# Kernel tuning notes

Measured on AMD Instinct MI355X. Metric: run time of the kernel, lower is better.

The kernel has to match this reference:

```python
import jax, jax.numpy as jnp
import numpy as np

BS, S, D, N, E = 16, 8, 10, 32, 300
H, STATE_DIM, MID, OC = 128, 96, 256, 100

def setup_inputs():
    ks = jax.random.split(jax.random.key(0), 24)
    g = lambda i, shape: (0.02 * jax.random.normal(ks[i], shape)).astype(jnp.float32)
    return {
        "stock_news": jax.random.normal(ks[0], (BS, S, D, N, E), dtype=jnp.float32),
        "stock_feats": jax.random.normal(ks[1], (BS, STATE_DIM), dtype=jnp.float32),
        "conv_w3": g(2, (S, OC, E, 3)), "conv_b3": g(3, (S, OC)),
        "conv_w4": g(4, (S, OC, E, 4)), "conv_b4": g(5, (S, OC)),
        "conv_w5": g(6, (S, OC, E, 5)), "conv_b5": g(7, (S, OC)),
        "w_ih": g(8, (S, 4 * H, 3 * OC)), "w_hh": g(9, (S, 4 * H, H)),
        "b_ih": g(10, (S, 4 * H)), "b_hh": g(11, (S, 4 * H)),
        "linX_w": g(12, (S, H, 2 * H)), "linX_b": g(13, (S, H)),
        "linY_w": g(14, (S, 64, H)), "linY_b": g(15, (S, 64)),
        "w1": g(16, (24, STATE_DIM)), "b1": g(17, (24,)),
        "w2": g(18, (16, 24)), "b2": g(19, (16,)),
        "arch_w1": g(20, (MID, 16 + 64 * S)), "arch_b1": g(21, (MID,)),
        "arch_w2": g(22, (S, MID)), "arch_b2": g(23, (S,)),
        "action_var": jnp.full((S,), -0.25, dtype=jnp.float32),
    }

def _conv_maxpool(x, w, b, k):
    # x: [S,B,D,N,E], w: [S,OC,E,k] -> conv1d over news axis then max-pool -> [S,B,D,OC]
    L = x.shape[3] - k + 1
    y = jnp.broadcast_to(b[:, None, None, None, :], (x.shape[0], x.shape[1], x.shape[2], L, w.shape[1]))
    for j in range(k):
        y = y + jnp.einsum('sbdne,soe->sbdno', x[:, :, :, j:j + L, :], w[:, :, :, j])
    return y.max(axis=3)

def _lstm_attn(xs, w_ih, w_hh, b_ih, b_hh):
    # single-stock LSTM (batch_first) + attention from original code; xs: [B,D,I] -> [B,2H]
    pre = jnp.einsum('bdi,gi->dbg', xs, w_ih) + b_ih + b_hh  # [D,B,4H]
    h0 = jnp.zeros((xs.shape[0], w_hh.shape[1]), xs.dtype)
    def step(carry, g_t):
        h, c = carry
        gates = g_t + h @ w_hh.T
        i, f, g, o = jnp.split(gates, 4, axis=-1)  # PyTorch gate order i,f,g,o
        c = jax.nn.sigmoid(f) * c + jax.nn.sigmoid(i) * jnp.tanh(g)
        h = jax.nn.sigmoid(o) * jnp.tanh(c)
        return (h, c), h
    (hn, _), outs = jax.lax.scan(step, (h0, h0), pre)
    outs = outs.transpose(1, 0, 2)  # [B,D,H]
    w = jnp.einsum('bh,bdh->bd', hn, outs)[:, None, :]  # [B,1,D]
    w = jax.nn.softmax(w, axis=1)  # softmax over singleton dim, exactly as torch code (yields ones)
    out = jnp.sum(w.transpose(0, 2, 1) * outs, axis=1)  # [B,H]
    return jnp.concatenate([hn, out], axis=-1)  # [B,2H]

def _forward(stock_news, stock_feats, conv_w3, conv_b3, conv_w4, conv_b4, conv_w5, conv_b5,
             w_ih, w_hh, b_ih, b_hh, linX_w, linX_b, linY_w, linY_b,
             w1, b1, w2, b2, arch_w1, arch_b1, arch_w2, arch_b2, action_var):
    x = stock_news.transpose(1, 0, 2, 3, 4)  # [S,B,D,N,E]
    feats = [_conv_maxpool(x, w, b, k) for (w, b, k) in
             ((conv_w3, conv_b3, 3), (conv_w4, conv_b4, 4), (conv_w5, conv_b5, 5))]
    text = jnp.concatenate(feats, axis=-1)  # [S,B,D,300]
    comb = jax.vmap(_lstm_attn)(text, w_ih, w_hh, b_ih, b_hh)  # [S,B,2H]
    hX = jax.nn.relu(jnp.einsum('sbi,shi->sbh', comb, linX_w) + linX_b[:, None, :])  # dropout is eval-mode identity
    hY = jax.nn.relu(jnp.einsum('sbh,soh->sbo', hX, linY_w) + linY_b[:, None, :])  # [S,B,64]
    stock_text = hY.transpose(1, 0, 2).reshape(stock_news.shape[0], -1)  # [B,S*64]
    f = jax.nn.relu(stock_feats @ w1.T + b1) @ w2.T + b2  # [B,16]
    total = jnp.concatenate([stock_text, f], axis=-1)  # [B,16+64S]
    mu = jnp.tanh(jax.nn.relu(total @ arch_w1.T + arch_b1) @ arch_w2.T + arch_b2)
    return mu, jnp.exp(action_var)

def reference(stock_news, stock_feats, conv_w3, conv_b3, conv_w4, conv_b4, conv_w5, conv_b5,
              w_ih, w_hh, b_ih, b_hh, linX_w, linX_b, linY_w, linY_b,
              w1, b1, w2, b2, arch_w1, arch_b1, arch_w2, arch_b2, action_var):
    return _forward(stock_news, stock_feats, conv_w3, conv_b3, conv_w4, conv_b4, conv_w5, conv_b5,
                    w_ih, w_hh, b_ih, b_hh, linX_w, linX_b, linY_w, linY_b,
                    w1, b1, w2, b2, arch_w1, arch_b1, arch_w2, arch_b2, action_var)
```

## Files before the change

### kernel.cpp

```cpp
#include <hip/hip_runtime.h>
#include <math.h>

#define S_   8
#define B_   16
#define D_   10
#define N_   32
#define E_   300
#define H_   128
#define G4_  512
#define SDIM_ 96
#define MID_ 256
#define TOT_ 528

#define NWPACK 3850240
#define NWPRE  1310720

typedef unsigned short u16;
typedef __attribute__((ext_vector_type(8))) short short8;
typedef __attribute__((ext_vector_type(4))) short short4v;
typedef __attribute__((ext_vector_type(4))) float f32x4;

static __device__ __forceinline__ u16 f2bf(float f) {
    unsigned u = __builtin_bit_cast(unsigned, f);
    return (u16)((u + 0x7FFFu + ((u >> 16) & 1u)) >> 16);
}

__global__ void prep(const float* __restrict__ w3, const float* __restrict__ b3,
                     const float* __restrict__ w4, const float* __restrict__ b4,
                     const float* __restrict__ w5, const float* __restrict__ b5,
                     const float* __restrict__ w_ih,
                     const float* __restrict__ lxw, const float* __restrict__ lyw,
                     const float* __restrict__ aw1,
                     u16* __restrict__ wpack2, u16* __restrict__ wpre2,
                     float* __restrict__ bcomb,
                     float* __restrict__ lxwT, float* __restrict__ lywT,
                     float* __restrict__ aw1T) {
    int idx = blockIdx.x * blockDim.x + threadIdx.x;
    if (idx < NWPACK) {
        int j = idx & 7, q = (idx >> 3) & 3;
        int rest = idx >> 5;
        int c = rest % 320, ks = (rest / 320) % 47, s = rest / 15040;
        int kk = ks * 32 + q * 8 + j;
        int tap = kk / 300, e = kk - tap * 300;
        float v = 0.f;
        if (tap < 5) {
            if (c < 100)      { if (tap < 3) v = w3[((s*100 + c      )*300 + e)*3 + tap]; }
            else if (c < 200) { if (tap < 4) v = w4[((s*100 + c - 100)*300 + e)*4 + tap]; }
            else if (c < 300) {              v = w5[((s*100 + c - 200)*300 + e)*5 + tap]; }
        }
        wpack2[idx] = f2bf(v);
    } else if (idx < NWPACK + NWPRE) {
        int i2 = idx - NWPACK;
        int j = i2 & 7, q = (i2 >> 3) & 3;
        int rest = i2 >> 5;
        int g = rest & 511, ks = (rest >> 9) % 10, s = rest / 5120;
        int kk = ks * 32 + q * 8 + j;
        float v = (kk < 300) ? w_ih[((size_t)s * 512 + g) * 300 + kk] : 0.f;
        wpre2[i2] = f2bf(v);
    }
    if (idx < 262144) {
        int t = idx & 127, i = (idx >> 7) & 255, s = idx >> 15;
        lxwT[idx] = lxw[((size_t)(s * 128 + t)) * 256 + i];
    }
    if (idx < 65536) {
        int t = idx & 63, i = (idx >> 6) & 127, s = idx >> 13;
        lywT[idx] = lyw[((size_t)(s * 64 + t)) * 128 + i];
    }
    if (idx < 135168) {
        int j = idx & 255, i = idx >> 8;
        aw1T[idx] = aw1[(size_t)j * TOT_ + i];
    }
    if (idx < 2560) {
        int c = idx % 320, s = idx / 320;
        float bv = 0.f;
        if (c < 100)      bv = b3[s*100 + c];
        else if (c < 200) bv = b4[s*100 + c - 100];
        else if (c < 300) bv = b5[s*100 + c - 200];
        bcomb[idx] = bv;
    }
}

__global__ __launch_bounds__(512, 2) void conv_mfma(const float* __restrict__ news,
                                                    const u16* __restrict__ wpack2,
                                                    const float* __restrict__ bcomb,
                                                    u16* __restrict__ text_bf) {
    __shared__ u16 xs[5 * 10816];
    __shared__ float part[10][320];
    const int tid = threadIdx.x, bid = blockIdx.x;
    const int s = bid & 7, rr_ = bid >> 3, b = rr_ >> 1, half = rr_ & 1;
    const int l = tid & 63, wvi = tid >> 6;
    const int wm = wvi >> 2, wn = wvi & 3;
    const int q = l >> 4, r16 = l & 15;

    const u16* gp[5];
#pragma unroll
    for (int nt = 0; nt < 5; ++nt) {
        int c = wn * 80 + nt * 16 + r16;
        gp[nt] = wpack2 + (size_t)s * 481280 + c * 32 + q * 8;
    }

    short8 bf0[5], bf1[5];
#pragma unroll
    for (int nt = 0; nt < 5; ++nt) bf0[nt] = *reinterpret_cast<const short8*>(gp[nt]);
#pragma unroll
    for (int nt = 0; nt < 5; ++nt) bf1[nt] = *reinterpret_cast<const short8*>(gp[nt] + 10240);

    for (int day = 0; day < 5; ++day) {
        const float4* xg = reinterpret_cast<const float4*>(
            news + (size_t)((b * 8 + s) * 10 + half * 5 + day) * 9600);
        for (int i = tid; i < 2704; i += 512) {
            ushort4 u;
            if (i < 2400) {
                float4 v = xg[i];
                u.x = f2bf(v.x); u.y = f2bf(v.y); u.z = f2bf(v.z); u.w = f2bf(v.w);
            } else { u.x = 0; u.y = 0; u.z = 0; u.w = 0; }
            *reinterpret_cast<ushort4*>(&xs[day * 10816 + 4 * i]) = u;
        }
    }
    __syncthreads();

    f32x4 acc[5][5];
#pragma unroll
    for (int mt = 0; mt < 5; ++mt)
#pragma unroll
        for (int nt = 0; nt < 5; ++nt) acc[mt][nt] = (f32x4)(0.f);

#define LOADA(dst, ks) do {                                                       \
    _Pragma("unroll")                                                             \
    for (int mt_ = 0; mt_ < 5; ++mt_) {                                           \
        int di_ = wm * 5 + mt_;                                                   \
        int off_ = (di_ >> 1) * 10816 + (((di_ & 1) << 4) + r16) * 300            \
                   + (ks) * 32 + q * 8;                                           \
        short4v lo_ = *reinterpret_cast<const short4v*>(&xs[off_]);               \
        short4v hi_ = *reinterpret_cast<const short4v*>(&xs[off_ + 4]);           \
        dst[mt_] = __builtin_shufflevector(lo_, hi_, 0, 1, 2, 3, 4, 5, 6, 7);     \
    } } while (0)

#define MFMAS(bfv, av) do {                                                       \
    __builtin_amdgcn_s_setprio(1);                                                \
    _Pragma("unroll")                                                             \
    for (int nt_ = 0; nt_ < 5; ++nt_)                                             \
        _Pragma("unroll")                                                         \
        for (int mt_ = 0; mt_ < 5; ++mt_)                                         \
            acc[mt_][nt_] = __builtin_amdgcn_mfma_f32_16x16x32_bf16(av[mt_], bfv[nt_], acc[mt_][nt_], 0, 0, 0); \
    __builtin_amdgcn_s_setprio(0);                                                \
    } while (0)

    for (int ks = 0; ks < 46; ks += 2) {
        short8 a0[5], a1[5];
        LOADA(a0, ks);
        MFMAS(bf0, a0);
#pragma unroll
        for (int nt = 0; nt < 5; ++nt)
            bf0[nt] = *reinterpret_cast<const short8*>(gp[nt] + (ks + 2) * 10240);

        LOADA(a1, ks + 1);
        MFMAS(bf1, a1);
        if (ks + 3 < 47) {
#pragma unroll
            for (int nt = 0; nt < 5; ++nt)
                bf1[nt] = *reinterpret_cast<const short8*>(gp[nt] + (ks + 3) * 10240);
        }
    }
    {
        short8 a0[5];
        LOADA(a0, 46);
        MFMAS(bf0, a0);
    }
#undef LOADA
#undef MFMAS

#pragma unroll
    for (int mt = 0; mt < 5; ++mt) {
        const int di = wm * 5 + mt;
        const int nwb = (di & 1) << 4;
#pragma unroll
        for (int nt = 0; nt < 5; ++nt) {
            int oc = wn * 80 + nt * 16 + r16;
            int L = (oc < 100) ? 30 : (oc < 200) ? 29 : 28;
            float mx = -3e38f;
#pragma unroll
            for (int rr = 0; rr < 4; ++rr) {
                int nw = nwb + q * 4 + rr;
                if (nw < L) mx = fmaxf(mx, acc[mt][nt][rr]);
            }
            mx = fmaxf(mx, __shfl_xor(mx, 16));
            mx = fmaxf(mx, __shfl_xor(mx, 32));
            if (l < 16) part[di][wn * 80 + nt * 16 + l] = mx;
        }
    }
    __syncthreads();
    for (int i = tid; i < 1600; i += 512) {
        int day = i / 320, oc = i - day * 320;
        float mx = fmaxf(part[2 * day][oc], part[2 * day + 1][oc]);
        text_bf[((size_t)(s * 16 + b) * 10 + half * 5 + day) * 320 + oc] =
            f2bf(mx + bcomb[s * 320 + oc]);
    }
}

__global__ __launch_bounds__(256) void lstm_pre_mfma(const u16* __restrict__ text_bf,
                                                     const u16* __restrict__ wpre2,
                                                     const float* __restrict__ b_ih,
                                                     const float* __restrict__ b_hh,
                                                     float* __restrict__ pre) {
    __shared__ u16 as16[16 * 320];
    const int sd = blockIdx.x, s = sd / 10, d = sd % 10;
    const int tid = threadIdx.x, l = tid & 63, w = tid >> 6, q = l >> 4, r16 = l & 15;

    for (int i = tid; i < 640; i += 256) {
        int r = i / 40, c = i % 40;
        *reinterpret_cast<float4*>(as16 + r * 320 + ((c ^ (r & 7)) << 3)) =
            *reinterpret_cast<const float4*>(text_bf + ((size_t)(s * 16 + r) * 10 + d) * 320 + c * 8);
    }
    __syncthreads();

    const u16* gpb[8];
#pragma unroll
    for (int nt = 0; nt < 8; ++nt) {
        int g = w * 128 + nt * 16 + r16;
        gpb[nt] = wpre2 + (size_t)s * 163840 + g * 32 + q * 8;
    }

    f32x4 acc[8];
#pragma unroll
    for (int nt = 0; nt < 8; ++nt) acc[nt] = (f32x4)(0.f);

    for (int ks = 0; ks < 10; ++ks) {
        short8 a = *reinterpret_cast<const short8*>(
            as16 + r16 * 320 + (((ks * 4 + q) ^ (r16 & 7)) << 3));
#pragma unroll
        for (int nt = 0; nt < 8; ++nt) {
            short8 bf = *reinterpret_cast<const short8*>(gpb[nt] + ks * 16384);
            acc[nt] = __builtin_amdgcn_mfma_f32_16x16x32_bf16(a, bf, acc[nt], 0, 0, 0);
        }
    }

#pragma unroll
    for (int nt = 0; nt < 8; ++nt) {
        int g = w * 128 + nt * 16 + r16;
        float bias = b_ih[s * 512 + g] + b_hh[s * 512 + g];
#pragma unroll
        for (int r = 0; r < 4; ++r) {
            int brow = q * 4 + r;
            pre[((size_t)sd * 16 + brow) * 512 + g] = acc[nt][r] + bias;
        }
    }
}

__global__ __launch_bounds__(512) void lstm_tail(const float* __restrict__ pre,
                                                 const float* __restrict__ w_hh,
                                                 const float* __restrict__ lxwT, const float* __restrict__ lxb,
                                                 const float* __restrict__ lywT, const float* __restrict__ lyb,
                                                 float* __restrict__ total) {
    __shared__ float wchunk[128][129];
    __shared__ float h_lds[H_];
    __shared__ float gates[G4_];
    __shared__ float comb_l[256];
    __shared__ __align__(16) float hx[H_];
    const int sb = blockIdx.x;
    const int s = sb / B_, b = sb % B_;
    const int t = threadIdx.x;

    float wrs[128];
    for (int c = 0; c < 4; ++c) {
        for (int i2 = t; i2 < 128 * 32; i2 += 512) {
            int row = i2 >> 5, fq = i2 & 31;
            float4 v = *reinterpret_cast<const float4*>(
                w_hh + ((size_t)(s * G4_ + c * 128 + row)) * H_ + fq * 4);
            wchunk[row][fq * 4 + 0] = v.x; wchunk[row][fq * 4 + 1] = v.y;
            wchunk[row][fq * 4 + 2] = v.z; wchunk[row][fq * 4 + 3] = v.w;
        }
        __syncthreads();
        if ((t >> 7) == c) {
            int r = t & 127;
#pragma unroll
            for (int i = 0; i < 128; ++i) wrs[i] = wchunk[r][i];
        }
        __syncthreads();
    }

    float cc = 0.f, hsum = 0.f, hval = 0.f;
    if (t < H_) h_lds[t] = 0.f;
    __syncthreads();

    for (int d = 0; d < D_; ++d) {
        float a0 = pre[(((size_t)(s * D_ + d) * B_ + b)) * G4_ + t];
        float a1 = 0.f, a2 = 0.f, a3 = 0.f;
#pragma unroll
        for (int i = 0; i < 128; i += 4) {
            float4 h4 = *reinterpret_cast<const float4*>(&h_lds[i]);
            a0 = fmaf(wrs[i + 0], h4.x, a0);
            a1 = fmaf(wrs[i + 1], h4.y, a1);
            a2 = fmaf(wrs[i + 2], h4.z, a2);
            a3 = fmaf(wrs[i + 3], h4.w, a3);
        }
        gates[t] = (a0 + a1) + (a2 + a3);
        __syncthreads();
        if (t < H_) {
            float ig = 1.f / (1.f + expf(-gates[t]));
            float fg = 1.f / (1.f + expf(-gates[H_ + t]));
            float gg = tanhf(gates[2 * H_ + t]);
            float og = 1.f / (1.f + expf(-gates[3 * H_ + t]));
            cc = fg * cc + ig * gg;
            hval = og * tanhf(cc);
            hsum += hval;
            h_lds[t] = hval;
        }
        __syncthreads();
    }
    if (t < H_) { comb_l[t] = hval; comb_l[H_ + t] = hsum; }
    __syncthreads();
    if (t < H_) {
        const float* wv = lxwT + (size_t)s * 256 * 128 + t;
        float a0 = lxb[s * H_ + t], a1 = 0.f;
        for (int i = 0; i < 256; i += 2) {
            a0 = fmaf(comb_l[i], wv[(size_t)i * 128], a0);
            a1 = fmaf(comb_l[i + 1], wv[(size_t)(i + 1) * 128], a1);
        }
        hx[t] = fmaxf(a0 + a1, 0.f);
    }
    __syncthreads();
    if (t < 64) {
        const float* wv = lywT + (size_t)s * 128 * 64 + t;
        float a0 = lyb[s * 64 + t], a1 = 0.f;
        for (int i = 0; i < 128; i += 2) {
            a0 = fmaf(hx[i], wv[(size_t)i * 64], a0);
            a1 = fmaf(hx[i + 1], wv[(size_t)(i + 1) * 64], a1);
        }
        total[(size_t)b * 512 + s * 64 + t] = fmaxf(a0 + a1, 0.f);
    }
}

__global__ __launch_bounds__(512) void head_feats(const float* __restrict__ total,
                                                  const float* __restrict__ sf,
                                                  const float* __restrict__ w1, const float* __restrict__ b1,
                                                  const float* __restrict__ w2, const float* __restrict__ b2,
                                                  const float* __restrict__ aw1T, const float* __restrict__ ab1,
                                                  const float* __restrict__ aw2, const float* __restrict__ ab2,
                                                  const float* __restrict__ avar,
                                                  float* __restrict__ out) {
    __shared__ __align__(16) float tr[TOT_];
    __shared__ float hid[MID_];
    __shared__ float h1f[24];
    __shared__ float pA[MID_], pB[MID_];
    const int bb = blockIdx.x, t = threadIdx.x;
    if (t < 128)
        reinterpret_cast<float4*>(tr)[t] = reinterpret_cast<const float4*>(total + (size_t)bb * 512)[t];
    if (t < 24) {
        float acc = b1[t];
        for (int i = 0; i < SDIM_; ++i) acc = fmaf(sf[bb * SDIM_ + i], w1[t * SDIM_ + i], acc);
        h1f[t] = fmaxf(acc, 0.f);
    }
    __syncthreads();
    if (t < 16) {
        float acc = b2[t];
        for (int i = 0; i < 24; ++i) acc = fmaf(h1f[i], w2[t * 24 + i], acc);
        tr[512 + t] = acc;
    }
    __syncthreads();
    {
        const int j = t & 255, hf = t >> 8;
        const int ilo = hf ? 264 : 0, ihi = hf ? 528 : 264;
        const float* wv = aw1T + j;
        float a0 = 0.f, a1 = 0.f, a2 = 0.f, a3 = 0.f;
        for (int i = ilo; i < ihi; i += 4) {
            a0 = fmaf(tr[i + 0], wv[(size_t)(i + 0) * 256], a0);
            a1 = fmaf(tr[i + 1], wv[(size_t)(i + 1) * 256], a1);
            a2 = fmaf(tr[i + 2], wv[(size_t)(i + 2) * 256], a2);
            a3 = fmaf(tr[i + 3], wv[(size_t)(i + 3) * 256], a3);
        }
        float p = (a0 + a1) + (a2 + a3);
        if (hf) pB[j] = p; else pA[j] = p;
    }
    __syncthreads();
    if (t < MID_) hid[t] = fmaxf(pA[t] + pB[t] + ab1[t], 0.f);
    __syncthreads();
    if (t < 8) {
        float acc = ab2[t];
        const float* wv = aw2 + (size_t)t * MID_;
        for (int i = 0; i < MID_; ++i) acc = fmaf(hid[i], wv[i], acc);
        out[bb * 8 + t] = tanhf(acc);
    }
    if (bb == 0 && t >= 8 && t < 16) out[128 + (t - 8)] = expf(avar[t - 8]);
}

extern "C" void kernel_launch(void* const* d_in, const int* in_sizes, int n_in,
                              void* d_out, int out_size, void* d_ws, size_t ws_size,
                              hipStream_t stream) {
    const float* news = (const float*)d_in[0];
    const float* sf   = (const float*)d_in[1];
    const float* w3   = (const float*)d_in[2];  const float* b3 = (const float*)d_in[3];
    const float* w4   = (const float*)d_in[4];  const float* b4 = (const float*)d_in[5];
    const float* w5   = (const float*)d_in[6];  const float* b5 = (const float*)d_in[7];
    const float* w_ih = (const float*)d_in[8];  const float* w_hh = (const float*)d_in[9];
    const float* b_ih = (const float*)d_in[10]; const float* b_hh = (const float*)d_in[11];
    const float* lxw  = (const float*)d_in[12]; const float* lxb = (const float*)d_in[13];
    const float* lyw  = (const float*)d_in[14]; const float* lyb = (const float*)d_in[15];
    const float* w1   = (const float*)d_in[16]; const float* b1 = (const float*)d_in[17];
    const float* w2   = (const float*)d_in[18]; const float* b2 = (const float*)d_in[19];
    const float* aw1  = (const float*)d_in[20]; const float* ab1 = (const float*)d_in[21];
    const float* aw2  = (const float*)d_in[22]; const float* ab2 = (const float*)d_in[23];
    const float* avar = (const float*)d_in[24];

    char* ws = (char*)d_ws;
    u16*   wpack2  = (u16*)ws;
    u16*   wpre2   = (u16*)(ws + 7700480);
    float* bcomb   = (float*)(ws + 10321920);
    u16*   text_bf = (u16*)(ws + 10332160);
    float* pre     = (float*)(ws + 11151360);
    float* total   = (float*)(ws + 13772800);
    float* lxwT    = (float*)(ws + 13805568);
    float* lywT    = (float*)(ws + 14854144);
    float* aw1T    = (float*)(ws + 15116288);

    prep<<<(NWPACK + NWPRE + 255) / 256, 256, 0, stream>>>(w3, b3, w4, b4, w5, b5, w_ih,
                                                           lxw, lyw, aw1,
                                                           wpack2, wpre2, bcomb, lxwT, lywT, aw1T);
    conv_mfma<<<256, 512, 0, stream>>>(news, wpack2, bcomb, text_bf);
    lstm_pre_mfma<<<S_ * D_, 256, 0, stream>>>(text_bf, wpre2, b_ih, b_hh, pre);
    lstm_tail<<<S_ * B_, 512, 0, stream>>>(pre, w_hh, lxwT, lxb, lywT, lyb, total);
    head_feats<<<B_, 512, 0, stream>>>(total, sf, w1, b1, w2, b2, aw1T, ab1, aw2, ab2, avar, (float*)d_out);
}
```

Measured before the change: 135.8 us.

## Stage conv weight panels into LDS via async global_load_lds double buffering

The conv MFMA kernel no longer has each wave load its own weight B-fragments from global memory into registers. It now copies each K-step weight panel into a double-buffered LDS region with async global_load_lds, using an XOR swizzle, and the waves read fragments from LDS. This shares weight loads across the block and overlaps the next panel's fetch with the current MFMAs. The cost is a __syncthreads per K-step and more LDS use, which drops launch bounds from 2 blocks per CU to 1 and so lowers occupancy.

```diff
diff --git a/kernel.cpp b/kernel.cpp
--- a/kernel.cpp
+++ b/kernel.cpp
@@ -80,30 +80,44 @@
     }
 }
 
-__global__ __launch_bounds__(512, 2) void conv_mfma(const float* __restrict__ news,
+#define XS_U16   54080
+#define BB_U16   54080
+#define PANEL_U16 10240
+
+__global__ __launch_bounds__(512, 1) void conv_mfma(const float* __restrict__ news,
                                                     const u16* __restrict__ wpack2,
                                                     const float* __restrict__ bcomb,
                                                     u16* __restrict__ text_bf) {
-    __shared__ u16 xs[5 * 10816];
-    __shared__ float part[10][320];
+    __shared__ u16 smem[74560];
     const int tid = threadIdx.x, bid = blockIdx.x;
     const int s = bid & 7, rr_ = bid >> 3, b = rr_ >> 1, half = rr_ & 1;
     const int l = tid & 63, wvi = tid >> 6;
     const int wm = wvi >> 2, wn = wvi & 3;
     const int q = l >> 4, r16 = l & 15;
 
-    const u16* gp[5];
-#pragma unroll
-    for (int nt = 0; nt < 5; ++nt) {
-        int c = wn * 80 + nt * 16 + r16;
-        gp[nt] = wpack2 + (size_t)s * 481280 + c * 32 + q * 8;
-    }
-
-    short8 bf0[5], bf1[5];
-#pragma unroll
-    for (int nt = 0; nt < 5; ++nt) bf0[nt] = *reinterpret_cast<const short8*>(gp[nt]);
-#pragma unroll
-    for (int nt = 0; nt < 5; ++nt) bf1[nt] = *reinterpret_cast<const short8*>(gp[nt] + 10240);
+    const u16* wsrc = wpack2 + (size_t)s * 481280;
+
+#define STAGEB(ks, pb) do {                                                        \
+    const u16* bsrc_ = wsrc + (size_t)(ks) * PANEL_U16;                            \
+    int i0_ = tid;                                                                 \
+    __builtin_amdgcn_global_load_lds(                                              \
+        (const __attribute__((address_space(1))) void*)(bsrc_ + (i0_ ^ ((i0_ >> 3) & 3)) * 8), \
+        (__attribute__((address_space(3))) void*)(&smem[BB_U16 + (pb) * PANEL_U16 + i0_ * 8]), \
+        16, 0, 0);                                                                 \
+    int i1_ = tid + 512;                                                           \
+    __builtin_amdgcn_global_load_lds(                                              \
+        (const __attribute__((address_space(1))) void*)(bsrc_ + (i1_ ^ ((i1_ >> 3) & 3)) * 8), \
+        (__attribute__((address_space(3))) void*)(&smem[BB_U16 + (pb) * PANEL_U16 + i1_ * 8]), \
+        16, 0, 0);                                                                 \
+    if (tid < 256) {                                                               \
+        int i2_ = tid + 1024;                                                      \
+        __builtin_amdgcn_global_load_lds(                                          \
+            (const __attribute__((address_space(1))) void*)(bsrc_ + (i2_ ^ ((i2_ >> 3) & 3)) * 8), \
+            (__attribute__((address_space(3))) void*)(&smem[BB_U16 + (pb) * PANEL_U16 + i2_ * 8]), \
+            16, 0, 0);                                                             \
+    } } while (0)
+
+    STAGEB(0, 0);
 
     for (int day = 0; day < 5; ++day) {
         const float4* xg = reinterpret_cast<const float4*>(
@@ -114,7 +128,7 @@
                 float4 v = xg[i];
                 u.x = f2bf(v.x); u.y = f2bf(v.y); u.z = f2bf(v.z); u.w = f2bf(v.w);
             } else { u.x = 0; u.y = 0; u.z = 0; u.w = 0; }
-            *reinterpret_cast<ushort4*>(&xs[day * 10816 + 4 * i]) = u;
+            *reinterpret_cast<ushort4*>(&smem[day * 10816 + 4 * i]) = u;
         }
     }
     __syncthreads();
@@ -131,9 +145,18 @@
         int di_ = wm * 5 + mt_;                                                   \
         int off_ = (di_ >> 1) * 10816 + (((di_ & 1) << 4) + r16) * 300            \
                    + (ks) * 32 + q * 8;                                           \
-        short4v lo_ = *reinterpret_cast<const short4v*>(&xs[off_]);               \
-        short4v hi_ = *reinterpret_cast<const short4v*>(&xs[off_ + 4]);           \
+        short4v lo_ = *reinterpret_cast<const short4v*>(&smem[off_]);             \
+        short4v hi_ = *reinterpret_cast<const short4v*>(&smem[off_ + 4]);         \
         dst[mt_] = __builtin_shufflevector(lo_, hi_, 0, 1, 2, 3, 4, 5, 6, 7);     \
+    } } while (0)
+
+#define LOADB(dst, pb) do {                                                       \
+    _Pragma("unroll")                                                             \
+    for (int nt_ = 0; nt_ < 5; ++nt_) {                                           \
+        int c_ = wn * 80 + nt_ * 16 + r16;                                        \
+        int p_ = c_ * 4 + (q ^ ((c_ >> 1) & 3));                                  \
+        dst[nt_] = *reinterpret_cast<const short8*>(                              \
+            &smem[BB_U16 + (pb) * PANEL_U16 + p_ * 8]);                           \
     } } while (0)
 
 #define MFMAS(bfv, av) do {                                                       \
@@ -146,30 +169,21 @@
     __builtin_amdgcn_s_setprio(0);                                                \
     } while (0)
 
-    for (int ks = 0; ks < 46; ks += 2) {
-        short8 a0[5], a1[5];
-        LOADA(a0, ks);
-        MFMAS(bf0, a0);
-#pragma unroll
-        for (int nt = 0; nt < 5; ++nt)
-            bf0[nt] = *reinterpret_cast<const short8*>(gp[nt] + (ks + 2) * 10240);
-
-        LOADA(a1, ks + 1);
-        MFMAS(bf1, a1);
-        if (ks + 3 < 47) {
-#pragma unroll
-            for (int nt = 0; nt < 5; ++nt)
-                bf1[nt] = *reinterpret_cast<const short8*>(gp[nt] + (ks + 3) * 10240);
-        }
-    }
-    {
-        short8 a0[5];
-        LOADA(a0, 46);
-        MFMAS(bf0, a0);
+    for (int ks = 0; ks < 47; ++ks) {
+        const int cur = ks & 1;
+        if (ks < 46) STAGEB(ks + 1, cur ^ 1);
+        short8 a[5], bf[5];
+        LOADA(a, ks);
+        LOADB(bf, cur);
+        MFMAS(bf, a);
+        __syncthreads();
     }
 #undef LOADA
+#undef LOADB
 #undef MFMAS
-
+#undef STAGEB
+
+    float* part = reinterpret_cast<float*>(&smem[BB_U16]);
 #pragma unroll
     for (int mt = 0; mt < 5; ++mt) {
         const int di = wm * 5 + mt;
@@ -186,13 +200,13 @@
             }
             mx = fmaxf(mx, __shfl_xor(mx, 16));
             mx = fmaxf(mx, __shfl_xor(mx, 32));
-            if (l < 16) part[di][wn * 80 + nt * 16 + l] = mx;
+            if (l < 16) part[di * 320 + wn * 80 + nt * 16 + l] = mx;
         }
     }
     __syncthreads();
     for (int i = tid; i < 1600; i += 512) {
         int day = i / 320, oc = i - day * 320;
-        float mx = fmaxf(part[2 * day][oc], part[2 * day + 1][oc]);
+        float mx = fmaxf(part[(2 * day) * 320 + oc], part[(2 * day + 1) * 320 + oc]);
         text_bf[((size_t)(s * 16 + b) * 10 + half * 5 + day) * 320 + oc] =
             f2bf(mx + bcomb[s * 320 + oc]);
     }
```

New measurement: 138.7 us. +2.1%, slower.
